# Optimization experiments

Hardware: AMD Instinct MI355X
Metric: run time of the kernel (lower is better)

Reference implementation:

```python
import jax, jax.numpy as jnp
import numpy as np

N = 2048   # num_params = feature dim = number of ring Givens angles
B = 16384  # batch


def setup_inputs() -> dict:
    key = jax.random.key(0)
    k1, k2 = jax.random.split(key)
    x = jax.random.normal(k1, (B, N), dtype=jnp.float32)
    angles = jax.random.normal(k2, (N,), dtype=jnp.float32)
    return {"x": x, "angles": angles}


def _build_rotation(angles):
    """R = G_0 @ G_1 @ ... @ G_{n-1}, built by sequential right-multiplication.

    Right-multiplying M by Givens G_k (plane (i, j)=(k, (k+1)%n), angle theta_k,
    with G[i,i]=c, G[j,i]=s, G[i,j]=-s, G[j,j]=c) only mixes columns i and j:
        new_col_i =  c*col_i + s*col_j
        new_col_j = -s*col_i + c*col_j
    This is O(n) per step -> O(n^2) total, identical math to the original
    O(n^4) loop of full n x n matmuls against per-step identity matrices.
    """
    n = angles.shape[0]
    idx_i = jnp.arange(n)
    idx_j = (idx_i + 1) % n

    def step(M, inp):
        theta, i, j = inp
        c = jnp.cos(theta)
        s = jnp.sin(theta)
        col_i = M[:, i]
        col_j = M[:, j]
        M = M.at[:, i].set(c * col_i + s * col_j)
        M = M.at[:, j].set(-s * col_i + c * col_j)
        return M, None

    M0 = jnp.eye(n, dtype=angles.dtype)
    R, _ = jax.lax.scan(step, M0, (angles, idx_i, idx_j))
    return R


def reference(x, angles):
    R = _build_rotation(angles)   # [N, N], orthogonal (product of Givens)
    return x @ R.T                # [B, N]
```

## Files before the change

### kernel.cpp

```cpp
#include <hip/hip_runtime.h>
#include <stdint.h>

#define NN  2048

__global__ void cs_init_kernel(const float* __restrict__ angles, float2* __restrict__ cs) {
    const int i = blockIdx.x * blockDim.x + threadIdx.x;
    if (i < NN) {
        float s, c;
        sincosf(angles[i], &s, &c);
        cs[i] = make_float2(c, s);
    }
}

__global__ __launch_bounds__(256, 4) void ring_rows_kernel(
        const float* __restrict__ x,
        const float2* __restrict__ cs,
        float* __restrict__ y,
        int B) {
    __shared__ float tuLds[4];
    __shared__ float eeLds[4];
    const int tid  = threadIdx.x;
    const int lane = tid & 63;
    const int wv   = tid >> 6;

    float qc[8], qs[8];
    {
        const float4* cs4 = (const float4*)cs + tid * 4;
        #pragma unroll
        for (int h = 0; h < 4; ++h) {
            float4 v = cs4[h];
            qc[2*h] = v.x; qs[2*h] = v.y; qc[2*h+1] = v.z; qs[2*h+1] = v.w;
        }
    }
    const float2 csl = cs[NN - 1];
    const float clv = csl.x, slv = csl.y;

    float Mt = ((qs[0]*qs[1])*(qs[2]*qs[3])) * ((qs[4]*qs[5])*(qs[6]*qs[7]));
    float Ms[6];
    float Mc = Mt;
    #pragma unroll
    for (int d = 1, st = 0; d < 64; d <<= 1, ++st) {
        Ms[st] = (lane + d < 64) ? Mc : 0.0f;
        float Mo = __shfl_down(Mc, d);
        if (lane + d < 64) Mc *= Mo;
    }
    float MexW = __shfl_down(Mc, 1);
    if (lane == 63) MexW = 1.0f;
    const float Tm = __shfl(Mc, 0);
    if (lane == 0) tuLds[wv] = Tm;
    __syncthreads();
    const float Tm1 = tuLds[1], Tm2 = tuLds[2], Tm3 = tuLds[3];
    __syncthreads();
    const float k1 = (wv == 0) ? 1.0f : 0.0f;
    const float k2 = (wv == 0) ? Tm1  : (wv == 1 ? 1.0f : 0.0f);
    const float k3 = (wv == 0) ? Tm1 * Tm2 : (wv == 1 ? Tm2 : (wv == 2 ? 1.0f : 0.0f));
    const float TmAbove = (wv == 0) ? Tm1 * Tm2 * Tm3
                        : (wv == 1) ? Tm2 * Tm3
                        : (wv == 2) ? Tm3 : 1.0f;
    const float Gm = MexW * TmAbove;

    int row = blockIdx.x;
    if (row >= B) return;
    float4 wa, wb; float x0, xl;
    {
        const float* xr = x + (size_t)row * NN;
        wa = *(const float4*)(xr + 8 * tid);
        wb = *(const float4*)(xr + 8 * tid + 4);
        x0 = xr[0]; xl = xr[NN - 1];
    }

    while (true) {
        const int nrow = row + gridDim.x;
        const bool hasNext = (nrow < B);
        float4 waN, wbN; float x0N = 0.0f, xlN = 0.0f;
        if (hasNext) {
            const float* xn = x + (size_t)nrow * NN;
            waN = *(const float4*)(xn + 8 * tid);
            wbN = *(const float4*)(xn + 8 * tid + 4);
            x0N = xn[0]; xlN = xn[NN - 1];
        }

        if (tid == 0) wa.x = slv * xl + clv * x0;

        float U;
        U =      qc[7] * wb.w;
        U = fmaf(-qs[6], U, qc[6] * wb.z);
        U = fmaf(-qs[5], U, qc[5] * wb.y);
        U = fmaf(-qs[4], U, qc[4] * wb.x);
        U = fmaf(-qs[3], U, qc[3] * wa.w);
        U = fmaf(-qs[2], U, qc[2] * wa.z);
        U = fmaf(-qs[1], U, qc[1] * wa.y);
        U = fmaf(-qs[0], U, qc[0] * wa.x);

        #pragma unroll
        for (int d = 1, st = 0; d < 64; d <<= 1, ++st) {
            float Uo = __shfl_down(U, d);
            U = fmaf(Ms[st], Uo, U);
        }
        float UexW = __shfl_down(U, 1);
        if (lane == 63) UexW = 0.0f;
        if (lane == 0) tuLds[wv] = U;
        __syncthreads();
        float XU = k1 * tuLds[1];
        XU = fmaf(k2, tuLds[2], XU);
        XU = fmaf(k3, tuLds[3], XU);
        float a = fmaf(Gm, x0, fmaf(MexW, XU, UexW));

        float e7 = fmaf(qc[7], a, qs[7] * wb.w);  a = fmaf(-qs[7], a, qc[7] * wb.w);
        float e6 = fmaf(qc[6], a, qs[6] * wb.z);  a = fmaf(-qs[6], a, qc[6] * wb.z);
        float e5 = fmaf(qc[5], a, qs[5] * wb.y);  a = fmaf(-qs[5], a, qc[5] * wb.y);
        float e4 = fmaf(qc[4], a, qs[4] * wb.x);  a = fmaf(-qs[4], a, qc[4] * wb.x);
        float e3 = fmaf(qc[3], a, qs[3] * wa.w);  a = fmaf(-qs[3], a, qc[3] * wa.w);
        float e2 = fmaf(qc[2], a, qs[2] * wa.z);  a = fmaf(-qs[2], a, qc[2] * wa.z);
        float e1 = fmaf(qc[1], a, qs[1] * wa.y);  a = fmaf(-qs[1], a, qc[1] * wa.y);
        float e0 = fmaf(qc[0], a, qs[0] * wa.x);  a = fmaf(-qs[0], a, qc[0] * wa.x);

        float prev = __shfl_up(e7, 1);
        if (lane == 63) eeLds[wv] = e7;
        __syncthreads();
        if (lane == 0 && wv > 0) prev = eeLds[wv - 1];
        const float s0 = (tid == 0) ? a : prev;

        float* yr = y + (size_t)row * NN + 8 * tid;
        *(float4*)(yr)     = make_float4(s0, e0, e1, e2);
        *(float4*)(yr + 4) = make_float4(e3, e4, e5, e6);

        if (!hasNext) break;
        row = nrow;
        wa = waN; wb = wbN; x0 = x0N; xl = xlN;
    }
}

extern "C" void kernel_launch(void* const* d_in, const int* in_sizes, int n_in,
                              void* d_out, int out_size, void* d_ws, size_t ws_size,
                              hipStream_t stream) {
    const float* x      = (const float*)d_in[0];
    const float* angles = (const float*)d_in[1];
    float* y            = (float*)d_out;
    float2* cs          = (float2*)d_ws;

    const int B = in_sizes[0] / NN;

    hipLaunchKernelGGL(cs_init_kernel, dim3(8), dim3(256), 0, stream, angles, cs);

    const int blocks = 2048;
    hipLaunchKernelGGL(ring_rows_kernel, dim3(blocks), dim3(256), 0, stream,
                       x, (const float2*)cs, y, B);
}
```

Measured before the change: 242.8 us.

## Process two rows per block without persistent loop, recompute lane-0 boundary locally

Replaces the persistent grid-stride kernel, which prefetched the next row, with a non-persistent kernel that handles two independent rows per block across B/2 blocks. The two scans are interleaved to expose ILP. The second LDS exchange and barrier for the cross-wave boundary element are removed by having each wave's lane 0 recompute that value from the inclusive prefix and a neighbouring x and cs value. Occupancy hint goes to 8 blocks per CU. The cost is per-block setup (cs loads, the M prefix scan and a barrier) repeated for every pair of rows instead of being amortised over many rows.

```diff
diff --git a/kernel.cpp b/kernel.cpp
--- a/kernel.cpp
+++ b/kernel.cpp
@@ -1,7 +1,7 @@
 #include <hip/hip_runtime.h>
 #include <stdint.h>
 
-#define NN  2048
+#define NN 2048
 
 __global__ void cs_init_kernel(const float* __restrict__ angles, float2* __restrict__ cs) {
     const int i = blockIdx.x * blockDim.x + threadIdx.x;
@@ -12,16 +12,39 @@
     }
 }
 
-__global__ __launch_bounds__(256, 4) void ring_rows_kernel(
+__global__ __launch_bounds__(256, 8) void ring_rows2_kernel(
         const float* __restrict__ x,
         const float2* __restrict__ cs,
         float* __restrict__ y,
         int B) {
-    __shared__ float tuLds[4];
-    __shared__ float eeLds[4];
+    __shared__ float tmL[4];
+    __shared__ float tuL[2][4];
     const int tid  = threadIdx.x;
     const int lane = tid & 63;
     const int wv   = tid >> 6;
+
+    const int row0 = blockIdx.x * 2;
+    if (row0 >= B) return;
+    const int row1  = min(row0 + 1, B - 1);
+    const bool st1  = (row0 + 1 < B);
+
+    const float* __restrict__ xr0 = x + (size_t)row0 * NN;
+    const float* __restrict__ xr1 = x + (size_t)row1 * NN;
+
+    float4 wa0 = *(const float4*)(xr0 + 8 * tid);
+    float4 wb0 = *(const float4*)(xr0 + 8 * tid + 4);
+    float4 wa1 = *(const float4*)(xr1 + 8 * tid);
+    float4 wb1 = *(const float4*)(xr1 + 8 * tid + 4);
+    const float x00 = xr0[0];
+    const float x01 = xr1[0];
+
+    float xm10 = 0.0f, xm11 = 0.0f, cm1 = 0.0f, sm1 = 0.0f;
+    if (lane == 0 && wv > 0) {
+        xm10 = xr0[8 * tid - 1];
+        xm11 = xr1[8 * tid - 1];
+        float2 t = cs[8 * tid - 1];
+        cm1 = t.x; sm1 = t.y;
+    }
 
     float qc[8], qs[8];
     {
@@ -32,8 +55,6 @@
             qc[2*h] = v.x; qs[2*h] = v.y; qc[2*h+1] = v.z; qs[2*h+1] = v.w;
         }
     }
-    const float2 csl = cs[NN - 1];
-    const float clv = csl.x, slv = csl.y;
 
     float Mt = ((qs[0]*qs[1])*(qs[2]*qs[3])) * ((qs[4]*qs[5])*(qs[6]*qs[7]));
     float Ms[6];
@@ -44,90 +65,90 @@
         float Mo = __shfl_down(Mc, d);
         if (lane + d < 64) Mc *= Mo;
     }
+    const float Minc = Mc;
     float MexW = __shfl_down(Mc, 1);
     if (lane == 63) MexW = 1.0f;
-    const float Tm = __shfl(Mc, 0);
-    if (lane == 0) tuLds[wv] = Tm;
+    if (lane == 0) tmL[wv] = Minc;
     __syncthreads();
-    const float Tm1 = tuLds[1], Tm2 = tuLds[2], Tm3 = tuLds[3];
-    __syncthreads();
+    const float Tm1 = tmL[1], Tm2 = tmL[2], Tm3 = tmL[3];
     const float k1 = (wv == 0) ? 1.0f : 0.0f;
     const float k2 = (wv == 0) ? Tm1  : (wv == 1 ? 1.0f : 0.0f);
     const float k3 = (wv == 0) ? Tm1 * Tm2 : (wv == 1 ? Tm2 : (wv == 2 ? 1.0f : 0.0f));
     const float TmAbove = (wv == 0) ? Tm1 * Tm2 * Tm3
                         : (wv == 1) ? Tm2 * Tm3
                         : (wv == 2) ? Tm3 : 1.0f;
-    const float Gm = MexW * TmAbove;
 
-    int row = blockIdx.x;
-    if (row >= B) return;
-    float4 wa, wb; float x0, xl;
-    {
-        const float* xr = x + (size_t)row * NN;
-        wa = *(const float4*)(xr + 8 * tid);
-        wb = *(const float4*)(xr + 8 * tid + 4);
-        x0 = xr[0]; xl = xr[NN - 1];
+    if (tid == 0) {
+        float2 csl = cs[NN - 1];
+        wa0.x = csl.y * xr0[NN - 1] + csl.x * x00;
+        wa1.x = csl.y * xr1[NN - 1] + csl.x * x01;
     }
 
-    while (true) {
-        const int nrow = row + gridDim.x;
-        const bool hasNext = (nrow < B);
-        float4 waN, wbN; float x0N = 0.0f, xlN = 0.0f;
-        if (hasNext) {
-            const float* xn = x + (size_t)nrow * NN;
-            waN = *(const float4*)(xn + 8 * tid);
-            wbN = *(const float4*)(xn + 8 * tid + 4);
-            x0N = xn[0]; xlN = xn[NN - 1];
+    float U0, U1;
+    U0 =      qc[7] * wb0.w;                     U1 =      qc[7] * wb1.w;
+    U0 = fmaf(-qs[6], U0, qc[6] * wb0.z);        U1 = fmaf(-qs[6], U1, qc[6] * wb1.z);
+    U0 = fmaf(-qs[5], U0, qc[5] * wb0.y);        U1 = fmaf(-qs[5], U1, qc[5] * wb1.y);
+    U0 = fmaf(-qs[4], U0, qc[4] * wb0.x);        U1 = fmaf(-qs[4], U1, qc[4] * wb1.x);
+    U0 = fmaf(-qs[3], U0, qc[3] * wa0.w);        U1 = fmaf(-qs[3], U1, qc[3] * wa1.w);
+    U0 = fmaf(-qs[2], U0, qc[2] * wa0.z);        U1 = fmaf(-qs[2], U1, qc[2] * wa1.z);
+    U0 = fmaf(-qs[1], U0, qc[1] * wa0.y);        U1 = fmaf(-qs[1], U1, qc[1] * wa1.y);
+    U0 = fmaf(-qs[0], U0, qc[0] * wa0.x);        U1 = fmaf(-qs[0], U1, qc[0] * wa1.x);
+
+    #pragma unroll
+    for (int d = 1, st = 0; d < 64; d <<= 1, ++st) {
+        float Uo0 = __shfl_down(U0, d);
+        float Uo1 = __shfl_down(U1, d);
+        U0 = fmaf(Ms[st], Uo0, U0);
+        U1 = fmaf(Ms[st], Uo1, U1);
+    }
+    float Ux0 = __shfl_down(U0, 1);
+    float Ux1 = __shfl_down(U1, 1);
+    if (lane == 63) { Ux0 = 0.0f; Ux1 = 0.0f; }
+    if (lane == 0) { tuL[0][wv] = U0; tuL[1][wv] = U1; }
+    __syncthreads();
+    float XU0 = k1 * tuL[0][1];  XU0 = fmaf(k2, tuL[0][2], XU0);  XU0 = fmaf(k3, tuL[0][3], XU0);
+    float XU1 = k1 * tuL[1][1];  XU1 = fmaf(k2, tuL[1][2], XU1);  XU1 = fmaf(k3, tuL[1][3], XU1);
+    const float h0 = fmaf(TmAbove, x00, XU0);
+    const float h1 = fmaf(TmAbove, x01, XU1);
+    float a0 = fmaf(MexW, h0, Ux0);
+    float a1 = fmaf(MexW, h1, Ux1);
+    const float aP0 = fmaf(Minc, h0, U0);
+    const float aP1 = fmaf(Minc, h1, U1);
+
+    float e70 = fmaf(qc[7], a0, qs[7]*wb0.w);  a0 = fmaf(-qs[7], a0, qc[7]*wb0.w);
+    float e71 = fmaf(qc[7], a1, qs[7]*wb1.w);  a1 = fmaf(-qs[7], a1, qc[7]*wb1.w);
+    float e60 = fmaf(qc[6], a0, qs[6]*wb0.z);  a0 = fmaf(-qs[6], a0, qc[6]*wb0.z);
+    float e61 = fmaf(qc[6], a1, qs[6]*wb1.z);  a1 = fmaf(-qs[6], a1, qc[6]*wb1.z);
+    float e50 = fmaf(qc[5], a0, qs[5]*wb0.y);  a0 = fmaf(-qs[5], a0, qc[5]*wb0.y);
+    float e51 = fmaf(qc[5], a1, qs[5]*wb1.y);  a1 = fmaf(-qs[5], a1, qc[5]*wb1.y);
+    float e40 = fmaf(qc[4], a0, qs[4]*wb0.x);  a0 = fmaf(-qs[4], a0, qc[4]*wb0.x);
+    float e41 = fmaf(qc[4], a1, qs[4]*wb1.x);  a1 = fmaf(-qs[4], a1, qc[4]*wb1.x);
+    float e30 = fmaf(qc[3], a0, qs[3]*wa0.w);  a0 = fmaf(-qs[3], a0, qc[3]*wa0.w);
+    float e31 = fmaf(qc[3], a1, qs[3]*wa1.w);  a1 = fmaf(-qs[3], a1, qc[3]*wa1.w);
+    float e20 = fmaf(qc[2], a0, qs[2]*wa0.z);  a0 = fmaf(-qs[2], a0, qc[2]*wa0.z);
+    float e21 = fmaf(qc[2], a1, qs[2]*wa1.z);  a1 = fmaf(-qs[2], a1, qc[2]*wa1.z);
+    float e10 = fmaf(qc[1], a0, qs[1]*wa0.y);  a0 = fmaf(-qs[1], a0, qc[1]*wa0.y);
+    float e11 = fmaf(qc[1], a1, qs[1]*wa1.y);  a1 = fmaf(-qs[1], a1, qc[1]*wa1.y);
+    float e00 = fmaf(qc[0], a0, qs[0]*wa0.x);  a0 = fmaf(-qs[0], a0, qc[0]*wa0.x);
+    float e01 = fmaf(qc[0], a1, qs[0]*wa1.x);  a1 = fmaf(-qs[0], a1, qc[0]*wa1.x);
+
+    float s00 = __shfl_up(e70, 1);
+    float s01 = __shfl_up(e71, 1);
+    if (lane == 0) {
+        if (wv == 0) { s00 = a0; s01 = a1; }
+        else {
+            s00 = fmaf(cm1, aP0, sm1 * xm10);
+            s01 = fmaf(cm1, aP1, sm1 * xm11);
         }
+    }
 
-        if (tid == 0) wa.x = slv * xl + clv * x0;
-
-        float U;
-        U =      qc[7] * wb.w;
-        U = fmaf(-qs[6], U, qc[6] * wb.z);
-        U = fmaf(-qs[5], U, qc[5] * wb.y);
-        U = fmaf(-qs[4], U, qc[4] * wb.x);
-        U = fmaf(-qs[3], U, qc[3] * wa.w);
-        U = fmaf(-qs[2], U, qc[2] * wa.z);
-        U = fmaf(-qs[1], U, qc[1] * wa.y);
-        U = fmaf(-qs[0], U, qc[0] * wa.x);
-
-        #pragma unroll
-        for (int d = 1, st = 0; d < 64; d <<= 1, ++st) {
-            float Uo = __shfl_down(U, d);
-            U = fmaf(Ms[st], Uo, U);
-        }
-        float UexW = __shfl_down(U, 1);
-        if (lane == 63) UexW = 0.0f;
-        if (lane == 0) tuLds[wv] = U;
-        __syncthreads();
-        float XU = k1 * tuLds[1];
-        XU = fmaf(k2, tuLds[2], XU);
-        XU = fmaf(k3, tuLds[3], XU);
-        float a = fmaf(Gm, x0, fmaf(MexW, XU, UexW));
-
-        float e7 = fmaf(qc[7], a, qs[7] * wb.w);  a = fmaf(-qs[7], a, qc[7] * wb.w);
-        float e6 = fmaf(qc[6], a, qs[6] * wb.z);  a = fmaf(-qs[6], a, qc[6] * wb.z);
-        float e5 = fmaf(qc[5], a, qs[5] * wb.y);  a = fmaf(-qs[5], a, qc[5] * wb.y);
-        float e4 = fmaf(qc[4], a, qs[4] * wb.x);  a = fmaf(-qs[4], a, qc[4] * wb.x);
-        float e3 = fmaf(qc[3], a, qs[3] * wa.w);  a = fmaf(-qs[3], a, qc[3] * wa.w);
-        float e2 = fmaf(qc[2], a, qs[2] * wa.z);  a = fmaf(-qs[2], a, qc[2] * wa.z);
-        float e1 = fmaf(qc[1], a, qs[1] * wa.y);  a = fmaf(-qs[1], a, qc[1] * wa.y);
-        float e0 = fmaf(qc[0], a, qs[0] * wa.x);  a = fmaf(-qs[0], a, qc[0] * wa.x);
-
-        float prev = __shfl_up(e7, 1);
-        if (lane == 63) eeLds[wv] = e7;
-        __syncthreads();
-        if (lane == 0 && wv > 0) prev = eeLds[wv - 1];
-        const float s0 = (tid == 0) ? a : prev;
-
-        float* yr = y + (size_t)row * NN + 8 * tid;
-        *(float4*)(yr)     = make_float4(s0, e0, e1, e2);
-        *(float4*)(yr + 4) = make_float4(e3, e4, e5, e6);
-
-        if (!hasNext) break;
-        row = nrow;
-        wa = waN; wb = wbN; x0 = x0N; xl = xlN;
+    float* yr0 = y + (size_t)row0 * NN + 8 * tid;
+    *(float4*)(yr0)     = make_float4(s00, e00, e10, e20);
+    *(float4*)(yr0 + 4) = make_float4(e30, e40, e50, e60);
+    if (st1) {
+        float* yr1 = y + (size_t)row1 * NN + 8 * tid;
+        *(float4*)(yr1)     = make_float4(s01, e01, e11, e21);
+        *(float4*)(yr1 + 4) = make_float4(e31, e41, e51, e61);
     }
 }
 
@@ -143,7 +164,7 @@
 
     hipLaunchKernelGGL(cs_init_kernel, dim3(8), dim3(256), 0, stream, angles, cs);
 
-    const int blocks = 2048;
-    hipLaunchKernelGGL(ring_rows_kernel, dim3(blocks), dim3(256), 0, stream,
+    const int blocks = (B + 1) / 2;
+    hipLaunchKernelGGL(ring_rows2_kernel, dim3(blocks), dim3(256), 0, stream,
                        x, (const float2*)cs, y, B);
 }
```

New measurement: 260.2 us. +7.2%, slower.
